# Kernel tuning notes

Hardware: AMD Instinct MI355X
Metric: run time of the kernel (lower is better)

## Reference

```python
import jax, jax.numpy as jnp
import numpy as np

N_TOKEN = 4096
INPUT_DIM = 1024
QUERY_DIM = 1024
VALUE_DIM = 1024


def setup_inputs() -> dict:
    key = jax.random.key(0)
    ks = jax.random.split(key, 7)
    s = 0.02
    return {
        "x": jax.random.normal(ks[0], (N_TOKEN, INPUT_DIM), dtype=jnp.float32),
        "W_q": jax.random.normal(ks[1], (INPUT_DIM, QUERY_DIM), dtype=jnp.float32) * s,
        "b_q": jax.random.normal(ks[2], (QUERY_DIM,), dtype=jnp.float32) * s,
        "W_k": jax.random.normal(ks[3], (INPUT_DIM, QUERY_DIM), dtype=jnp.float32) * s,
        "b_k": jax.random.normal(ks[4], (QUERY_DIM,), dtype=jnp.float32) * s,
        "W_v": jax.random.normal(ks[5], (INPUT_DIM, VALUE_DIM), dtype=jnp.float32) * s,
        "b_v": jax.random.normal(ks[6], (VALUE_DIM,), dtype=jnp.float32) * s,
    }


def reference(x, W_q, b_q, W_k, b_k, W_v, b_v):
    # Projections: [n, d_in] @ [d_in, d_q/v]
    Q = x @ W_q + b_q
    K = x @ W_k + b_k
    V = x @ W_v + b_v
    n, q_dim = Q.shape
    scale = 1.0 / jnp.sqrt(jnp.asarray(q_dim, dtype=Q.dtype))
    scores = (Q @ K.T) * scale  # [n, n]
    # causal mask: positions j > i get -inf
    causal = jnp.tril(jnp.ones((n, n), dtype=bool))
    scores = jnp.where(causal, scores, -jnp.inf)
    attn = jax.nn.softmax(scores, axis=-1)
    return attn @ V
```

## Files before the change

kernel.cpp:

```cpp
#include <hip/hip_runtime.h>

#define N_TOK 4096
#define DIM   1024

typedef __bf16 bf16x8 __attribute__((ext_vector_type(8)));
typedef float  f32x4  __attribute__((ext_vector_type(4)));

__device__ __forceinline__ unsigned short f2bf(float f) {
  union { float f; unsigned u; } v; v.f = f;
  unsigned u = v.u;
  return (unsigned short)((u + 0x7fffu + ((u >> 16) & 1u)) >> 16);
}
__device__ __forceinline__ float bf2f(unsigned short h) {
  union { unsigned u; float f; } v; v.u = ((unsigned)h) << 16;
  return v.f;
}

__device__ __forceinline__ void gll16(const unsigned short* g,
                                      unsigned short* l) {
  __builtin_amdgcn_global_load_lds(
      (const __attribute__((address_space(1))) unsigned int*)g,
      (__attribute__((address_space(3))) unsigned int*)l, 16, 0, 0);
}

#define PB_CVT 0
#define PB_TQ 2048
#define PB_LSUM 5120
#define PB_BIAS 5124
#define PB_TOTAL 5127

__global__ void prep(const float* __restrict__ x, const float* __restrict__ Wq,
                     const float* __restrict__ Wk, const float* __restrict__ Wv,
                     const float* __restrict__ bq, const float* __restrict__ bk,
                     const float* __restrict__ bv,
                     unsigned short* __restrict__ xs,
                     unsigned short* __restrict__ Wt,
                     float* __restrict__ ball, float* __restrict__ Lsum) {
  const int b = blockIdx.x;
  const int t = threadIdx.x;
  if (b < PB_TQ) {
    const int i = ((b - PB_CVT) * 256 + t) * 8;
    float4 v0 = *(const float4*)(x + i);
    float4 v1 = *(const float4*)(x + i + 4);
    ushort4 r0, r1;
    r0.x = f2bf(v0.x); r0.y = f2bf(v0.y); r0.z = f2bf(v0.z); r0.w = f2bf(v0.w);
    r1.x = f2bf(v1.x); r1.y = f2bf(v1.y); r1.z = f2bf(v1.z); r1.w = f2bf(v1.w);
    *(ushort4*)(xs + i) = r0;
    *(ushort4*)(xs + i + 4) = r1;
  } else if (b < PB_LSUM) {
    const int which = (b - PB_TQ) >> 10;
    const int lb = (b - PB_TQ) & 1023;
    const float* W = (which == 0) ? Wq : (which == 1) ? Wk : Wv;
    unsigned short* D = Wt + (size_t)which * 1024 * 1024;
    __shared__ float tile[32][33];
    const int bx = (lb & 31) * 32, by = (lb >> 5) * 32;
    const int tx = t & 31, ty = t >> 5;
    for (int r = ty; r < 32; r += 8)
      tile[r][tx] = W[(size_t)(by + r) * DIM + bx + tx];
    __syncthreads();
    for (int r = ty; r < 32; r += 8)
      D[(size_t)(bx + r) * DIM + by + tx] = f2bf(tile[tx][r]);
  } else if (b < PB_BIAS) {
    const int i = ((b - PB_LSUM) * 256 + t) * 4;
    *(float4*)(Lsum + i) = make_float4(0.f, 0.f, 0.f, 0.f);
  } else {
    const int i = ((b - PB_BIAS) * 256 + t) * 4;
#pragma unroll
    for (int c = 0; c < 4; c++) {
      const int k = i + c;
      if (k < 3072)
        ball[k] = (k < 1024) ? bq[k] * 0.03125f
                             : ((k < 2048) ? bk[k - 1024] : bv[k - 2048]);
    }
  }
}

#define BK 64

template <int EPI>
__global__ void gemm_tn(const unsigned short* __restrict__ A,
                        const unsigned short* __restrict__ B,
                        void* __restrict__ Cout,
                        const float* __restrict__ bias,
                        float* __restrict__ Lsum,
                        unsigned short* __restrict__ VT,
                        float* __restrict__ Part,
                        int K, int lda, int ldb, int ldc) {
  int bm, bn, kbeg, kend;
  int zz = 0, pidx = 0;
  if (EPI == 3) {
    const int i = blockIdx.x;
    bn = i & 7;
    const int q = i >> 3;
    if (q < 8)       { bm = q;                    zz = 0; }
    else if (q < 24) { bm = 8 + ((q - 8) >> 1);   zz = (q - 8) & 1; }
    else if (q < 48) { bm = 16 + (q - 24) / 3;    zz = (q - 24) % 3; }
    else             { bm = 24 + ((q - 48) >> 2); zz = (q - 48) & 3; }
    const int Keff = (bm + 1) * 128;
    kbeg = zz * 1024;
    kend = min(kbeg + 1024, Keff);
    pidx = (bm < 16) ? (bm - 8)
         : (bm < 24) ? 8 + (bm - 16) * 2 + (zz - 1)
                     : 24 + (bm - 24) * 3 + (zz - 1);
  } else if (EPI == 2) {
    const int id = blockIdx.x;
    const int wg = (id & 7) * 66 + (id >> 3);
    float s = sqrtf(8.f * (float)wg + 1.f);
    bm = (int)((s - 1.f) * 0.5f);
    while ((bm + 1) * (bm + 2) / 2 <= wg) ++bm;
    while (bm * (bm + 1) / 2 > wg) --bm;
    bn = wg - bm * (bm + 1) / 2;
    kbeg = 0; kend = K;
  } else {
    const int id = blockIdx.y * gridDim.x + blockIdx.x;
    const int wg = (id & 7) * 96 + (id >> 3);
    bm = wg / 24; bn = wg % 24;
    kbeg = 0; kend = K;
  }

  __shared__ __align__(16) unsigned short smA[128 * 64];
  __shared__ __align__(16) unsigned short smB[128 * 64];

  const int t = threadIdx.x;
  const int lane = t & 63, w = t >> 6;
  const int wm = (w & 1) * 64, wn = (w >> 1) * 64;

  f32x4 acc[4][4] = {};

  const unsigned short* Ab = A + (size_t)bm * 128 * lda;
  const unsigned short* Bb = B + (size_t)bn * 128 * ldb;

  const int rA = wm + (lane & 15);
  const int rB = wn + (lane & 15);
  const int kquad = (lane >> 4) << 3;
  const int swz = (lane & 7) << 3;

  const int lr = lane >> 3;
  const int g8 = ((lane & 7) ^ lr) << 3;
  const unsigned short* pa = Ab + (size_t)lr * lda + g8 + kbeg;
  const unsigned short* pb = Bb + (size_t)lr * ldb + g8 + kbeg;

  for (int k0 = kbeg; k0 < kend; k0 += BK) {
    __syncthreads();
#pragma unroll
    for (int m = 0; m < 4; m++) {
      const int r0 = (w << 5) + (m << 3);
      gll16(pa + (size_t)r0 * lda, smA + r0 * 64);
      gll16(pb + (size_t)r0 * ldb, smB + r0 * 64);
    }
    pa += BK; pb += BK;
    __syncthreads();

#pragma unroll
    for (int kk = 0; kk < BK; kk += 32) {
      bf16x8 af[4], bfr[4];
      const int kof = (kk + kquad) ^ swz;
#pragma unroll
      for (int i = 0; i < 4; i++)
        af[i] = *(const bf16x8*)(&smA[(rA + i * 16) * 64 + kof]);
#pragma unroll
      for (int j = 0; j < 4; j++)
        bfr[j] = *(const bf16x8*)(&smB[(rB + j * 16) * 64 + kof]);
#pragma unroll
      for (int i = 0; i < 4; i++)
#pragma unroll
        for (int j = 0; j < 4; j++)
          acc[i][j] = __builtin_amdgcn_mfma_f32_16x16x32_bf16(af[i], bfr[j],
                                                              acc[i][j], 0, 0, 0);
    }
  }

  float* Cf = (float*)Cout;
  unsigned short* Ch = (unsigned short*)Cout;
  const int colbase = bn * 128 + wn + (lane & 15);
  const int rowbase = bm * 128 + wm + ((lane >> 4) << 2);

  if (EPI == 0) {
    const bool isV = (bn >= 16);
#pragma unroll
    for (int i = 0; i < 4; i++)
#pragma unroll
      for (int j = 0; j < 4; j++) {
        const int gc = colbase + j * 16;
        const float cs = (gc < 1024) ? 0.03125f : 1.0f;
        const float bs = bias[gc];
        ushort4 h4;
        unsigned short* hp = (unsigned short*)&h4;
#pragma unroll
        for (int r = 0; r < 4; r++) {
          const int gr = rowbase + i * 16 + r;
          const unsigned short h = f2bf(acc[i][j][r] * cs + bs);
          Ch[(size_t)gr * ldc + gc] = h;
          hp[r] = h;
        }
        if (isV) {
          const int gr0 = rowbase + i * 16;
          *(ushort4*)(VT + (size_t)(gc - 2048) * N_TOK + gr0) = h4;
        }
      }
  } else if (EPI == 2) {
    __syncthreads();
    float* Lp = (float*)smA;
    if (t < 128) Lp[t] = 0.f;
    __syncthreads();
#pragma unroll
    for (int i = 0; i < 4; i++)
#pragma unroll
      for (int r = 0; r < 4; r++) {
        const int gr = rowbase + i * 16 + r;
        float sj = 0.f;
#pragma unroll
        for (int j = 0; j < 4; j++) {
          const int gc = colbase + j * 16;
          unsigned short h = 0;
          if (gc <= gr) h = f2bf(__expf(acc[i][j][r]));
          Ch[(size_t)gr * ldc + gc] = h;
          sj += bf2f(h);
        }
        sj += __shfl_xor(sj, 1);
        sj += __shfl_xor(sj, 2);
        sj += __shfl_xor(sj, 4);
        sj += __shfl_xor(sj, 8);
        if ((lane & 15) == 0)
          atomicAdd(&Lp[wm + ((lane >> 4) << 2) + i * 16 + r], sj);
      }
    __syncthreads();
    if (t < 128) atomicAdd(&Lsum[bm * 128 + t], Lp[t]);
  } else {
    float* dst = (zz == 0) ? (Cf + (size_t)bm * 128 * 1024)
                           : (Part + (size_t)pidx * 131072);
    const int colloc = bn * 128 + wn + (lane & 15);
    const int rowloc = wm + ((lane >> 4) << 2);
#pragma unroll
    for (int i = 0; i < 4; i++)
#pragma unroll
      for (int r = 0; r < 4; r++) {
        const int rr = rowloc + i * 16 + r;
        const float linv = 1.0f / Lsum[bm * 128 + rr];
#pragma unroll
        for (int j = 0; j < 4; j++)
          dst[(size_t)rr * 1024 + colloc + j * 16] = acc[i][j][r] * linv;
      }
  }
}

__global__ void reduce_out(const float* __restrict__ Part,
                           float* __restrict__ out) {
  const int bm = 8 + blockIdx.x;
  const int sub = blockIdx.y;
  const int extra = (bm < 16) ? 1 : (bm < 24) ? 2 : 3;
  const int pbase = (bm < 16) ? (bm - 8)
                  : (bm < 24) ? 8 + (bm - 16) * 2
                              : 24 + (bm - 24) * 3;
  const int t = threadIdx.x;
  float4* po = (float4*)(out + (size_t)(bm * 128 + sub * 4) * 1024);
  const float4* pp = (const float4*)(Part + (size_t)pbase * 131072 +
                                     (size_t)sub * 4096);
#pragma unroll
  for (int k = 0; k < 4; k++) {
    const int idx = t + k * 256;
    float4 v = po[idx];
    for (int e = 0; e < extra; e++) {
      const float4 q = pp[(size_t)e * 32768 + idx];
      v.x += q.x; v.y += q.y; v.z += q.z; v.w += q.w;
    }
    po[idx] = v;
  }
}

extern "C" void kernel_launch(void* const* d_in, const int* in_sizes, int n_in,
                              void* d_out, int out_size, void* d_ws,
                              size_t ws_size, hipStream_t stream) {
  (void)in_sizes; (void)n_in; (void)out_size; (void)ws_size;
  const float* x  = (const float*)d_in[0];
  const float* Wq = (const float*)d_in[1];
  const float* bq = (const float*)d_in[2];
  const float* Wk = (const float*)d_in[3];
  const float* bk = (const float*)d_in[4];
  const float* Wv = (const float*)d_in[5];
  const float* bv = (const float*)d_in[6];
  float* out = (float*)d_out;

  const size_t M1 = (size_t)1024 * 1024;
  unsigned short* xb   = (unsigned short*)d_ws;
  unsigned short* Wt   = xb + 4 * M1;
  unsigned short* Call = Wt + 3 * M1;
  unsigned short* Sb   = Call + 12 * M1;
  float* ball          = (float*)(Sb + 16 * M1);
  float* Lsum          = ball + 3072;
  unsigned short* xs   = Sb;
  float* Part          = (float*)Wt;

  prep<<<PB_TOTAL, 256, 0, stream>>>(x, Wq, Wk, Wv, bq, bk, bv, xs, Wt,
                                     ball, Lsum);
  gemm_tn<0><<<dim3(24, 32), 256, 0, stream>>>(xs, Wt, Call, ball, nullptr,
                                               xb, nullptr, DIM, DIM, DIM,
                                               3 * DIM);
  gemm_tn<2><<<528, 256, 0, stream>>>(Call, Call + 1024, Sb, nullptr, Lsum,
                                      nullptr, nullptr, DIM, 3 * DIM, 3 * DIM,
                                      N_TOK);
  gemm_tn<3><<<640, 256, 0, stream>>>(Sb, xb, out, nullptr, Lsum, nullptr,
                                      Part, N_TOK, N_TOK, N_TOK, DIM);
  reduce_out<<<dim3(24, 32), 256, 0, stream>>>(Part, out);
}
```

Baseline: 184.8 us.

## Use 64x128 tiles with two-wave blocks for causal score GEMM

The causal QK^T score kernel now uses 64-row by 128-column tiles, launched as 1056 blocks of 128 threads instead of 528 blocks of 256 threads. The triangular tile-index decode is rewritten for the half-height row blocks, and the row-sum reduction is resized to match. The intent is finer load balancing across compute units and less wasted work in diagonal tiles. In exchange, each block reuses less data from LDS, since B tiles are loaded per 64 rows instead of per 128.

```diff
diff --git a/kernel.cpp b/kernel.cpp
--- a/kernel.cpp
+++ b/kernel.cpp
@@ -86,6 +86,8 @@
                         unsigned short* __restrict__ VT,
                         float* __restrict__ Part,
                         int K, int lda, int ldb, int ldc) {
+  constexpr int AROWS = (EPI == 2) ? 64 : 128;
+
   int bm, bn, kbeg, kend;
   int zz = 0, pidx = 0;
   if (EPI == 3) {
@@ -104,12 +106,12 @@
                      : 24 + (bm - 24) * 3 + (zz - 1);
   } else if (EPI == 2) {
     const int id = blockIdx.x;
-    const int wg = (id & 7) * 66 + (id >> 3);
-    float s = sqrtf(8.f * (float)wg + 1.f);
-    bm = (int)((s - 1.f) * 0.5f);
-    while ((bm + 1) * (bm + 2) / 2 <= wg) ++bm;
-    while (bm * (bm + 1) / 2 > wg) --bm;
-    bn = wg - bm * (bm + 1) / 2;
+    const int wg = (id & 7) * 132 + (id >> 3);
+    int k = (int)((sqrtf(4.f * (float)wg + 1.f) - 1.f) * 0.5f);
+    while ((k + 1) * (k + 2) <= wg) ++k;
+    while (k * (k + 1) > wg) --k;
+    if (wg < (k + 1) * (k + 1)) { bm = 2 * k;     bn = wg - k * (k + 1); }
+    else                        { bm = 2 * k + 1; bn = wg - (k + 1) * (k + 1); }
     kbeg = 0; kend = K;
   } else {
     const int id = blockIdx.y * gridDim.x + blockIdx.x;
@@ -118,16 +120,17 @@
     kbeg = 0; kend = K;
   }
 
-  __shared__ __align__(16) unsigned short smA[128 * 64];
+  __shared__ __align__(16) unsigned short smA[AROWS * 64];
   __shared__ __align__(16) unsigned short smB[128 * 64];
 
   const int t = threadIdx.x;
   const int lane = t & 63, w = t >> 6;
-  const int wm = (w & 1) * 64, wn = (w >> 1) * 64;
+  const int wm = (EPI == 2) ? 0 : (w & 1) * 64;
+  const int wn = (EPI == 2) ? w * 64 : (w >> 1) * 64;
 
   f32x4 acc[4][4] = {};
 
-  const unsigned short* Ab = A + (size_t)bm * 128 * lda;
+  const unsigned short* Ab = A + (size_t)bm * AROWS * lda;
   const unsigned short* Bb = B + (size_t)bn * 128 * ldb;
 
   const int rA = wm + (lane & 15);
@@ -146,7 +149,19 @@
     for (int m = 0; m < 4; m++) {
       const int r0 = (w << 5) + (m << 3);
       gll16(pa + (size_t)r0 * lda, smA + r0 * 64);
-      gll16(pb + (size_t)r0 * ldb, smB + r0 * 64);
+    }
+    if (EPI == 2) {
+#pragma unroll
+      for (int m = 0; m < 8; m++) {
+        const int r0 = (w << 6) + (m << 3);
+        gll16(pb + (size_t)r0 * ldb, smB + r0 * 64);
+      }
+    } else {
+#pragma unroll
+      for (int m = 0; m < 4; m++) {
+        const int r0 = (w << 5) + (m << 3);
+        gll16(pb + (size_t)r0 * ldb, smB + r0 * 64);
+      }
     }
     pa += BK; pb += BK;
     __syncthreads();
@@ -165,17 +180,17 @@
       for (int i = 0; i < 4; i++)
 #pragma unroll
         for (int j = 0; j < 4; j++)
-          acc[i][j] = __builtin_amdgcn_mfma_f32_16x16x32_bf16(af[i], bfr[j],
-                                                              acc[i][j], 0, 0, 0);
+          acc[i][j] = __builtin_amdgcn_mfma_f32_16x16x32_bf16(
+              af[i], bfr[j], acc[i][j], 0, 0, 0);
     }
   }
 
   float* Cf = (float*)Cout;
   unsigned short* Ch = (unsigned short*)Cout;
-  const int colbase = bn * 128 + wn + (lane & 15);
-  const int rowbase = bm * 128 + wm + ((lane >> 4) << 2);
+  const int rowbase = bm * AROWS + wm + ((lane >> 4) << 2);
 
   if (EPI == 0) {
+    const int colbase = bn * 128 + wn + (lane & 15);
     const bool isV = (bn >= 16);
 #pragma unroll
     for (int i = 0; i < 4; i++)
@@ -199,9 +214,10 @@
         }
       }
   } else if (EPI == 2) {
+    const int colbase = bn * 128 + wn + (lane & 15);
     __syncthreads();
     float* Lp = (float*)smA;
-    if (t < 128) Lp[t] = 0.f;
+    if (t < 64) Lp[t] = 0.f;
     __syncthreads();
 #pragma unroll
     for (int i = 0; i < 4; i++)
@@ -222,10 +238,10 @@
         sj += __shfl_xor(sj, 4);
         sj += __shfl_xor(sj, 8);
         if ((lane & 15) == 0)
-          atomicAdd(&Lp[wm + ((lane >> 4) << 2) + i * 16 + r], sj);
-      }
-    __syncthreads();
-    if (t < 128) atomicAdd(&Lsum[bm * 128 + t], Lp[t]);
+          atomicAdd(&Lp[((lane >> 4) << 2) + i * 16 + r], sj);
+      }
+    __syncthreads();
+    if (t < 64) atomicAdd(&Lsum[bm * 64 + t], Lp[t]);
   } else {
     float* dst = (zz == 0) ? (Cf + (size_t)bm * 128 * 1024)
                            : (Part + (size_t)pidx * 131072);
@@ -296,9 +312,9 @@
   gemm_tn<0><<<dim3(24, 32), 256, 0, stream>>>(xs, Wt, Call, ball, nullptr,
                                                xb, nullptr, DIM, DIM, DIM,
                                                3 * DIM);
-  gemm_tn<2><<<528, 256, 0, stream>>>(Call, Call + 1024, Sb, nullptr, Lsum,
-                                      nullptr, nullptr, DIM, 3 * DIM, 3 * DIM,
-                                      N_TOK);
+  gemm_tn<2><<<1056, 128, 0, stream>>>(Call, Call + 1024, Sb, nullptr, Lsum,
+                                       nullptr, nullptr, DIM, 3 * DIM, 3 * DIM,
+                                       N_TOK);
   gemm_tn<3><<<640, 256, 0, stream>>>(Sb, xb, out, nullptr, Lsum, nullptr,
                                       Part, N_TOK, N_TOK, N_TOK, DIM);
   reduce_out<<<dim3(24, 32), 256, 0, stream>>>(Part, out);
```

New measurement: 190.7 us. +3.2%, slower.
